# Optimization experiments

Hardware: AMD Instinct MI355X
Metric: run time of the kernel (lower is better)

## Reference

```python
import jax, jax.numpy as jnp
import numpy as np

N_POS, D_MODEL, D_SAE, TOP_K = 2, 1024, 32768, 32


def setup_inputs() -> dict:
    key = jax.random.key(0)
    k_x, k_we, k_wd = jax.random.split(key, 3)
    x = jax.random.normal(k_x, (4096, N_POS, D_MODEL), dtype=jnp.float32)
    W_enc = jax.random.normal(k_we, (N_POS, D_MODEL, D_SAE), dtype=jnp.float32) * (1.0 / D_MODEL ** 0.5)
    W_dec = jax.random.normal(k_wd, (D_SAE, N_POS, D_MODEL), dtype=jnp.float32) * (1.0 / D_SAE ** 0.5)
    b_enc = jnp.zeros((D_SAE,), dtype=jnp.float32)
    b_dec = jnp.zeros((N_POS, D_MODEL), dtype=jnp.float32)
    return {"x": x, "W_enc": W_enc, "W_dec": W_dec, "b_enc": b_enc, "b_dec": b_dec}


def reference(x, W_enc, W_dec, b_enc, b_dec):
    # Encode: per-position einsum then shared bias -> (batch, d_sae)
    pre_act = jnp.einsum('btd,tds->bs', x, W_enc) + b_enc
    top_vals, top_idx = jax.lax.top_k(pre_act, TOP_K)  # (b, k)
    batch = pre_act.shape[0]
    rows = jnp.arange(batch)[:, None]  # (b, 1) broadcast against (b, k)
    z = jnp.zeros_like(pre_act).at[rows, top_idx].set(jax.nn.relu(top_vals))
    # Decode: dense contraction over d_sae -> (batch, n_positions, d_model)
    x_hat = jnp.einsum('bs,std->btd', z, W_dec) + b_dec
    return x_hat
```

## Files before the change

kernel.cpp:

```cpp
#include <hip/hip_runtime.h>
#include <cstdint>
#include <cstddef>

typedef unsigned short u16;
typedef unsigned long long u64;
typedef __attribute__((ext_vector_type(8))) short short8;
typedef __attribute__((ext_vector_type(4))) float f32x4;

constexpr int K_DIM = 2048;
constexpr int S_DIM = 32768;
constexpr int TOPK  = 32;
constexpr int CAP   = 256;
#define EPS      0.06f
#define THR_EMIT 3.7f
#define HIST_LO  3.5f

__device__ __forceinline__ u16 f2bf(float f) {
    unsigned u = __float_as_uint(f);
    return (u16)((u + 0x7FFFu + ((u >> 16) & 1u)) >> 16);
}
__device__ __forceinline__ unsigned key_map(float f) {
    unsigned u = __float_as_uint(f);
    return (u & 0x80000000u) ? ~u : (u | 0x80000000u);
}
__device__ __forceinline__ float key_unmap(unsigned k) {
    unsigned u = (k & 0x80000000u) ? (k ^ 0x80000000u) : ~k;
    return __uint_as_float(u);
}

__global__ __launch_bounds__(256) void init_kernel(int* __restrict__ flag, int M)
{
    int i = blockIdx.x * 256 + threadIdx.x;
    if (i < M) flag[i] = 0;
}

__global__ __launch_bounds__(256) void conv_x_kernel(
    const float* __restrict__ x, u16* __restrict__ hi, int n4)
{
    int i = blockIdx.x * 256 + threadIdx.x;
    if (i >= n4) return;
    float4 v = ((const float4*)x)[i];
    ushort4 h;
    h.x = f2bf(v.x); h.y = f2bf(v.y); h.z = f2bf(v.z); h.w = f2bf(v.w);
    ((ushort4*)hi)[i] = h;
}

__global__ __launch_bounds__(256) void conv_wt_kernel(
    const float* __restrict__ W, float* __restrict__ WT, u16* __restrict__ Wh)
{
    __shared__ float tile[64][65];
    const int t  = threadIdx.x;
    const int s0 = blockIdx.x * 64;
    const int k0 = blockIdx.y * 64;
#pragma unroll
    for (int i = 0; i < 4; ++i) {
        int kl = (t >> 4) + i * 16;
        int sc = (t & 15) * 4;
        float4 v = *(const float4*)&W[(size_t)(k0 + kl) * S_DIM + s0 + sc];
        tile[kl][sc] = v.x; tile[kl][sc + 1] = v.y;
        tile[kl][sc + 2] = v.z; tile[kl][sc + 3] = v.w;
    }
    __syncthreads();
    const int klc = (t & 7) * 8;
#pragma unroll
    for (int i = 0; i < 2; ++i) {
        int sl = (t >> 3) + i * 32;
        float f[8];
        short8 h8;
#pragma unroll
        for (int j = 0; j < 8; ++j) {
            f[j] = tile[klc + j][sl];
            h8[j] = (short)f2bf(f[j]);
        }
        size_t o = (size_t)(s0 + sl) * K_DIM + k0 + klc;
        *(float4*)&WT[o]     = make_float4(f[0], f[1], f[2], f[3]);
        *(float4*)&WT[o + 4] = make_float4(f[4], f[5], f[6], f[7]);
        *(short8*)&Wh[o] = h8;
    }
}

__device__ __forceinline__ void gl16(const u16* g, u16* s) {
    __builtin_amdgcn_global_load_lds(
        (const __attribute__((address_space(1))) unsigned int*)g,
        (__attribute__((address_space(3))) unsigned int*)s,
        16, 0, 0);
}

#define LGKM0  do { asm volatile("s_waitcnt lgkmcnt(0)" ::: "memory"); \
                    __builtin_amdgcn_sched_barrier(0); } while (0)
#define VMW(n) asm volatile("s_waitcnt vmcnt(" #n ")" ::: "memory")
#define BAR    do { __builtin_amdgcn_s_barrier(); \
                    __builtin_amdgcn_sched_barrier(0); } while (0)

__global__ __launch_bounds__(512, 2) void gemm_mfma_kernel(
    const u16* __restrict__ A, const u16* __restrict__ B,
    const float* __restrict__ bias, float* __restrict__ C)
{
    __shared__ alignas(16) u16 sA[2][256 * 64];
    __shared__ alignas(16) u16 sB[2][256 * 64];

    const int t = threadIdx.x;
    const int lane = t & 63;
    const int w = t >> 6;
    const int wm = w >> 2, wn = w & 3;

    const int nwg = gridDim.x;
    const int q = nwg >> 3;
    const int bid = blockIdx.x;
    const int wg = (bid & 7) * q + (bid >> 3);
    const int bm = wg >> 7;
    const int bn = wg & 127;

    const u16* Ab = A + (size_t)bm * 256 * K_DIM;
    const u16* Bb = B + (size_t)bn * 256 * K_DIM;

    const int w2  = w * 2;
    const int lr3 = lane >> 3;
    const int csw = ((lane & 7) ^ lr3) * 8;

    const int rl = lane & 15, kq = lane >> 4;
    const int swz = rl & 7;
    const int ac0 = (kq ^ swz) * 8;
    const int ac1 = ((4 + kq) ^ swz) * 8;
    const int arow = (wm * 16 + rl) * 64;
    const int brow = (wn * 16 + rl) * 64;

    f32x4 acc[8][4];
#pragma unroll
    for (int m = 0; m < 8; ++m)
#pragma unroll
        for (int n = 0; n < 4; ++n) acc[m][n] = (f32x4){0.f, 0.f, 0.f, 0.f};

    auto stA = [&](int half, int j, int kt, int buf) {
        const u16* src = Ab + (size_t)(half * 128 + (w2 + j) * 8 + lr3) * K_DIM
                            + kt * 64 + csw;
        gl16(src, &sA[buf][half * 8192 + (w2 + j) * 512]);
    };
    auto stB = [&](int half, int j, int kt, int buf) {
        const u16* src = Bb + (size_t)(half * 128 + (w2 + j) * 8 + lr3) * K_DIM
                            + kt * 64 + csw;
        gl16(src, &sB[buf][half * 8192 + (w2 + j) * 512]);
    };

    stA(0, 0, 0, 0); stA(0, 1, 0, 0);
    stB(0, 0, 0, 0); stB(0, 1, 0, 0);
    stB(1, 0, 0, 0); stB(1, 1, 0, 0);
    stA(1, 0, 0, 0); stA(1, 1, 0, 0);
    VMW(4);
    BAR;

    short8 af[4][2], bf[4][2];

#pragma unroll 1
    for (int kt = 0; kt < 32; ++kt) {
        const int cur = kt & 1, nxt = cur ^ 1;
        const bool more = (kt < 31);

#pragma unroll
        for (int m = 0; m < 4; ++m) {
            af[m][0] = *(const short8*)&sA[cur][arow + m * 2048 + ac0];
            af[m][1] = *(const short8*)&sA[cur][arow + m * 2048 + ac1];
        }
#pragma unroll
        for (int n = 0; n < 2; ++n) {
            bf[n][0] = *(const short8*)&sB[cur][brow + n * 4096 + ac0];
            bf[n][1] = *(const short8*)&sB[cur][brow + n * 4096 + ac1];
        }
        if (more) { stA(0, 0, kt + 1, nxt); stA(0, 1, kt + 1, nxt); }
        __builtin_amdgcn_s_barrier();
        LGKM0;
        __builtin_amdgcn_s_setprio(1);
#pragma unroll
        for (int m = 0; m < 4; ++m)
#pragma unroll
            for (int n = 0; n < 2; ++n)
#pragma unroll
                for (int kk = 0; kk < 2; ++kk)
                    acc[m][n] = __builtin_amdgcn_mfma_f32_16x16x32_bf16(
                        af[m][kk], bf[n][kk], acc[m][n], 0, 0, 0);
        __builtin_amdgcn_s_setprio(0);
        if (more) VMW(4); else VMW(2);
        BAR;

#pragma unroll
        for (int n = 2; n < 4; ++n) {
            bf[n][0] = *(const short8*)&sB[cur][brow + n * 4096 + ac0];
            bf[n][1] = *(const short8*)&sB[cur][brow + n * 4096 + ac1];
        }
        if (more) { stB(0, 0, kt + 1, nxt); stB(0, 1, kt + 1, nxt); }
        __builtin_amdgcn_s_barrier();
        LGKM0;
        __builtin_amdgcn_s_setprio(1);
#pragma unroll
        for (int m = 0; m < 4; ++m)
#pragma unroll
            for (int n = 2; n < 4; ++n)
#pragma unroll
                for (int kk = 0; kk < 2; ++kk)
                    acc[m][n] = __builtin_amdgcn_mfma_f32_16x16x32_bf16(
                        af[m][kk], bf[n][kk], acc[m][n], 0, 0, 0);
        __builtin_amdgcn_s_setprio(0);
        if (more) VMW(4); else VMW(0);
        BAR;

#pragma unroll
        for (int m = 0; m < 4; ++m) {
            af[m][0] = *(const short8*)&sA[cur][arow + (m + 4) * 2048 + ac0];
            af[m][1] = *(const short8*)&sA[cur][arow + (m + 4) * 2048 + ac1];
        }
        if (more) { stB(1, 0, kt + 1, nxt); stB(1, 1, kt + 1, nxt); }
        __builtin_amdgcn_s_barrier();
        LGKM0;
        __builtin_amdgcn_s_setprio(1);
#pragma unroll
        for (int m = 0; m < 4; ++m)
#pragma unroll
            for (int n = 2; n < 4; ++n)
#pragma unroll
                for (int kk = 0; kk < 2; ++kk)
                    acc[m + 4][n] = __builtin_amdgcn_mfma_f32_16x16x32_bf16(
                        af[m][kk], bf[n][kk], acc[m + 4][n], 0, 0, 0);
        __builtin_amdgcn_s_setprio(0);
        BAR;

        if (more) { stA(1, 0, kt + 1, nxt); stA(1, 1, kt + 1, nxt); }
        __builtin_amdgcn_s_barrier();
        __builtin_amdgcn_s_setprio(1);
#pragma unroll
        for (int m = 0; m < 4; ++m)
#pragma unroll
            for (int n = 0; n < 2; ++n)
#pragma unroll
                for (int kk = 0; kk < 2; ++kk)
                    acc[m + 4][n] = __builtin_amdgcn_mfma_f32_16x16x32_bf16(
                        af[m][kk], bf[n][kk], acc[m + 4][n], 0, 0, 0);
        __builtin_amdgcn_s_setprio(0);
        if (more) VMW(4);
        BAR;
    }

    const int colB = bn * 256 + wn * 16 + rl;
    const size_t rowB = (size_t)bm * 256 + wm * 16 + kq * 4;
    float bv[4];
#pragma unroll
    for (int n = 0; n < 4; ++n) bv[n] = bias[colB + n * 64];
#pragma unroll
    for (int m = 0; m < 8; ++m)
#pragma unroll
        for (int n = 0; n < 4; ++n)
#pragma unroll
            for (int rr = 0; rr < 4; ++rr)
                C[(rowB + m * 32 + rr) * S_DIM + colB + n * 64] =
                    acc[m][n][rr] + bv[n];
}

__global__ __launch_bounds__(256) void screen_kernel(
    const float* __restrict__ pre, u64* __restrict__ emit,
    int* __restrict__ ccnt, float* __restrict__ thrv,
    int* __restrict__ flag, int row0)
{
    __shared__ unsigned hist[64];
    __shared__ int cnt;

    const int t = threadIdx.x;
    const int row = blockIdx.x;
    const int grow = row0 + row;
    const float* prow = pre + (size_t)row * S_DIM;

    if (t < 64) hist[t] = 0;
    if (t == 0) cnt = 0;
    __syncthreads();

    u64* erow = emit + (size_t)grow * CAP;
    for (int i = t * 4; i < S_DIM; i += 1024) {
        float4 v = *(const float4*)(prow + i);
        float vv[4] = {v.x, v.y, v.z, v.w};
#pragma unroll
        for (int j = 0; j < 4; ++j) {
            if (vv[j] >= HIST_LO) {
                int b = (int)((vv[j] - HIST_LO) * 25.0f);
                if (b > 63) b = 63;
                atomicAdd(&hist[b], 1u);
                if (vv[j] >= THR_EMIT) {
                    int p = atomicAdd(&cnt, 1);
                    if (p < CAP)
                        erow[p] = ((u64)key_map(vv[j]) << 32) | (unsigned)(i + j);
                }
            }
        }
    }
    __syncthreads();

    if (t == 0) {
        unsigned acc = 0;
        int b = -1;
        for (int j = 63; j >= 0; --j) {
            acc += hist[j];
            if (acc >= (unsigned)TOPK) { b = j; break; }
        }
        float thr = HIST_LO + 0.04f * b - 2.0f * EPS - 1e-4f;
        if (b < 0 || cnt > CAP || thr < THR_EMIT) {
            flag[grow] = 1;
            thr = THR_EMIT;
        }
        thrv[grow] = thr;
        ccnt[grow] = (cnt < CAP) ? cnt : CAP;
    }
}

__global__ __launch_bounds__(256) void rescore_kernel(
    const float* __restrict__ x, const float* __restrict__ WT,
    const float* __restrict__ benc, const u64* __restrict__ emit,
    const int* __restrict__ ccnt, const float* __restrict__ thrv,
    float* __restrict__ resc, int row0)
{
    const int row = row0 + blockIdx.x;
    const int t = threadIdx.x;
    const int w = t >> 6, l = t & 63;
    const int cnt = ccnt[row];
    const float thr = thrv[row];

    __shared__ float xs[K_DIM];
    const float* xr = x + (size_t)row * K_DIM;
    for (int i = t * 4; i < K_DIM; i += 1024)
        *(float4*)&xs[i] = *(const float4*)&xr[i];
    __syncthreads();

    for (int c = w; c < cnt; c += 4) {
        const u64 pk = emit[(size_t)row * CAP + c];
        const float approx = key_unmap((unsigned)(pk >> 32));
        if (approx < thr) {
            if (l == 0) resc[(size_t)row * CAP + c] = -3e38f;
            continue;
        }
        const int s = (int)(pk & 0xFFFFFFFFu);
        const float* wc = WT + (size_t)s * K_DIM;
        float acc = 0.f;
#pragma unroll
        for (int j = 0; j < 32; ++j)
            acc = fmaf(xs[l + 64 * j], wc[l + 64 * j], acc);
#pragma unroll
        for (int d = 1; d < 64; d <<= 1) acc += __shfl_xor(acc, d);
        if (l == 0) resc[(size_t)row * CAP + c] = acc + benc[s];
    }
}

__global__ __launch_bounds__(64) void select_kernel(
    const float* __restrict__ resc, const u64* __restrict__ emit,
    const int* __restrict__ ccnt, const float* __restrict__ thrv,
    float* __restrict__ tv, int* __restrict__ ti, int* __restrict__ flag,
    int row0)
{
    const int row = row0 + blockIdx.x;
    const int l = threadIdx.x;
    const int cnt = ccnt[row];

    float v[4] = {0.f, 0.f, 0.f, 0.f};
    int   s[4] = {-1, -1, -1, -1};
    u64   p[4] = {0, 0, 0, 0};
#pragma unroll
    for (int j = 0; j < 4; ++j) {
        int c = l + j * 64;
        if (c < cnt) {
            s[j] = (int)(emit[(size_t)row * CAP + c] & 0xFFFFFFFFu);
            v[j] = resc[(size_t)row * CAP + c];
            p[j] = ((u64)key_map(v[j]) << 32) | (unsigned)(~s[j]);
        }
    }

    float* tvr = tv + (size_t)row * TOPK;
    int*   tir = ti + (size_t)row * TOPK;
    float v32f = -3e38f;
#pragma unroll 1
    for (int r = 0; r < TOPK; ++r) {
        u64 m = p[0];
        if (p[1] > m) m = p[1];
        if (p[2] > m) m = p[2];
        if (p[3] > m) m = p[3];
#pragma unroll
        for (int d = 1; d < 64; d <<= 1) {
            u64 o = __shfl_xor(m, d);
            if (o > m) m = o;
        }
        if (r == TOPK - 1) v32f = key_unmap((unsigned)(m >> 32));
        if (p[0] == m)      { tvr[r] = v[0]; tir[r] = s[0] < 0 ? 0 : s[0]; p[0] = 0; }
        else if (p[1] == m) { tvr[r] = v[1]; tir[r] = s[1] < 0 ? 0 : s[1]; p[1] = 0; }
        else if (p[2] == m) { tvr[r] = v[2]; tir[r] = s[2] < 0 ? 0 : s[2]; p[2] = 0; }
        else if (p[3] == m) { tvr[r] = v[3]; tir[r] = s[3] < 0 ? 0 : s[3]; p[3] = 0; }
    }
    if (l == 0) {
        if (v32f < thrv[row] + EPS) flag[row] = 1;
    }
}

__global__ __launch_bounds__(256) void fb_screen_kernel(
    const float* __restrict__ pre, u64* __restrict__ emit,
    int* __restrict__ ccnt, const int* __restrict__ flag, int row0)
{
    const int grow = row0 + blockIdx.x;
    if (!flag[grow]) return;

    __shared__ unsigned hist[2048];
    __shared__ unsigned partial[256];
    __shared__ unsigned sh_tk;
    __shared__ int cnt;

    const int t = threadIdx.x;
    const float* prow = pre + (size_t)blockIdx.x * S_DIM;

    for (int i = t; i < 2048; i += 256) hist[i] = 0;
    if (t == 0) cnt = 0;
    __syncthreads();

    for (int i = t * 4; i < S_DIM; i += 1024) {
        float4 v = *(const float4*)(prow + i);
        unsigned k0 = key_map(v.x), k1 = key_map(v.y),
                 k2 = key_map(v.z), k3 = key_map(v.w);
        if (k0 >= 0xC0000000u) atomicAdd(&hist[(k0 >> 19) - 6144], 1u);
        if (k1 >= 0xC0000000u) atomicAdd(&hist[(k1 >> 19) - 6144], 1u);
        if (k2 >= 0xC0000000u) atomicAdd(&hist[(k2 >> 19) - 6144], 1u);
        if (k3 >= 0xC0000000u) atomicAdd(&hist[(k3 >> 19) - 6144], 1u);
    }
    __syncthreads();

    unsigned ps = 0;
#pragma unroll
    for (int j = 0; j < 8; ++j) ps += hist[t * 8 + j];
    partial[t] = ps;
    __syncthreads();

    if (t == 0) {
        unsigned acc = 0;
        int seg = -1;
        for (int s = 255; s >= 0; --s) {
            if (acc + partial[s] >= (unsigned)TOPK) { seg = s; break; }
            acc += partial[s];
        }
        int bucket = 6144;
        if (seg >= 0) {
            for (int b = seg * 8 + 7; b >= seg * 8; --b) {
                acc += hist[b];
                if (acc >= (unsigned)TOPK) { bucket = 6144 + b; break; }
            }
        }
        float lo = key_unmap(((unsigned)bucket) << 19) - 2.0f * EPS;
        sh_tk = key_map(lo);
    }
    __syncthreads();

    const unsigned TK = sh_tk;
    u64* erow = emit + (size_t)grow * CAP;
    for (int i = t * 4; i < S_DIM; i += 1024) {
        float4 v = *(const float4*)(prow + i);
        unsigned k[4] = {key_map(v.x), key_map(v.y), key_map(v.z), key_map(v.w)};
#pragma unroll
        for (int j = 0; j < 4; ++j)
            if (k[j] >= TK) {
                int p = atomicAdd(&cnt, 1);
                if (p < CAP) erow[p] = ((u64)k[j] << 32) | (unsigned)(i + j);
            }
    }
    __syncthreads();
    if (t == 0) ccnt[grow] = (cnt < CAP) ? cnt : CAP;
}

__global__ __launch_bounds__(256) void fb_rescore_kernel(
    const float* __restrict__ x, const float* __restrict__ WT,
    const float* __restrict__ benc, const u64* __restrict__ emit,
    const int* __restrict__ ccnt, float* __restrict__ resc,
    const int* __restrict__ flag, int row0)
{
    const int row = row0 + blockIdx.x;
    if (!flag[row]) return;
    const int t = threadIdx.x;
    const int w = t >> 6, l = t & 63;
    const int cnt = ccnt[row];

    __shared__ float xs[K_DIM];
    const float* xr = x + (size_t)row * K_DIM;
    for (int i = t * 4; i < K_DIM; i += 1024)
        *(float4*)&xs[i] = *(const float4*)&xr[i];
    __syncthreads();

    for (int c = w; c < cnt; c += 4) {
        const int s = (int)(emit[(size_t)row * CAP + c] & 0xFFFFFFFFu);
        const float* wc = WT + (size_t)s * K_DIM;
        float acc = 0.f;
#pragma unroll
        for (int j = 0; j < 32; ++j)
            acc = fmaf(xs[l + 64 * j], wc[l + 64 * j], acc);
#pragma unroll
        for (int d = 1; d < 64; d <<= 1) acc += __shfl_xor(acc, d);
        if (l == 0) resc[(size_t)row * CAP + c] = acc + benc[s];
    }
}

__global__ __launch_bounds__(64) void fb_select_kernel(
    const float* __restrict__ resc, const u64* __restrict__ emit,
    const int* __restrict__ ccnt, float* __restrict__ tv,
    int* __restrict__ ti, const int* __restrict__ flag, int row0)
{
    const int row = row0 + blockIdx.x;
    if (!flag[row]) return;
    const int l = threadIdx.x;
    const int cnt = ccnt[row];

    float v[4] = {0.f, 0.f, 0.f, 0.f};
    int   s[4] = {-1, -1, -1, -1};
    u64   p[4] = {0, 0, 0, 0};
#pragma unroll
    for (int j = 0; j < 4; ++j) {
        int c = l + j * 64;
        if (c < cnt) {
            s[j] = (int)(emit[(size_t)row * CAP + c] & 0xFFFFFFFFu);
            v[j] = resc[(size_t)row * CAP + c];
            p[j] = ((u64)key_map(v[j]) << 32) | (unsigned)(~s[j]);
        }
    }

    float* tvr = tv + (size_t)row * TOPK;
    int*   tir = ti + (size_t)row * TOPK;
#pragma unroll 1
    for (int r = 0; r < TOPK; ++r) {
        u64 m = p[0];
        if (p[1] > m) m = p[1];
        if (p[2] > m) m = p[2];
        if (p[3] > m) m = p[3];
#pragma unroll
        for (int d = 1; d < 64; d <<= 1) {
            u64 o = __shfl_xor(m, d);
            if (o > m) m = o;
        }
        if (p[0] == m)      { tvr[r] = v[0]; tir[r] = s[0] < 0 ? 0 : s[0]; p[0] = 0; }
        else if (p[1] == m) { tvr[r] = v[1]; tir[r] = s[1] < 0 ? 0 : s[1]; p[1] = 0; }
        else if (p[2] == m) { tvr[r] = v[2]; tir[r] = s[2] < 0 ? 0 : s[2]; p[2] = 0; }
        else if (p[3] == m) { tvr[r] = v[3]; tir[r] = s[3] < 0 ? 0 : s[3]; p[3] = 0; }
    }
}

__global__ __launch_bounds__(256) void decode_kernel(
    const float* __restrict__ tval, const int* __restrict__ tidx,
    const float* __restrict__ Wd, const float* __restrict__ bdec,
    float* __restrict__ out, int row0)
{
    const int row = row0 + blockIdx.x;
    const int t = threadIdx.x;
    __shared__ float sv[TOPK];
    __shared__ int   si[TOPK];
    if (t < TOPK) {
        sv[t] = fmaxf(tval[(size_t)row * TOPK + t], 0.f);
        si[t] = tidx[(size_t)row * TOPK + t];
    }
    __syncthreads();

    const int c0 = t * 4;
    float4 acc0 = *(const float4*)(bdec + c0);
    float4 acc1 = *(const float4*)(bdec + 1024 + c0);
#pragma unroll 4
    for (int i = 0; i < TOPK; ++i) {
        const float z = sv[i];
        if (z > 0.f) {
            const float* wr = Wd + (size_t)si[i] * K_DIM;
            float4 w0 = *(const float4*)(wr + c0);
            float4 w1 = *(const float4*)(wr + 1024 + c0);
            acc0.x = fmaf(z, w0.x, acc0.x); acc0.y = fmaf(z, w0.y, acc0.y);
            acc0.z = fmaf(z, w0.z, acc0.z); acc0.w = fmaf(z, w0.w, acc0.w);
            acc1.x = fmaf(z, w1.x, acc1.x); acc1.y = fmaf(z, w1.y, acc1.y);
            acc1.z = fmaf(z, w1.z, acc1.z); acc1.w = fmaf(z, w1.w, acc1.w);
        }
    }
    float* op = out + (size_t)row * K_DIM;
    *(float4*)(op + c0) = acc0;
    *(float4*)(op + 1024 + c0) = acc1;
}

extern "C" void kernel_launch(void* const* d_in, const int* in_sizes, int n_in,
                              void* d_out, int out_size, void* d_ws, size_t ws_size,
                              hipStream_t stream)
{
    const float* x     = (const float*)d_in[0];
    const float* W_enc = (const float*)d_in[1];
    const float* W_dec = (const float*)d_in[2];
    const float* b_enc = (const float*)d_in[3];
    const float* b_dec = (const float*)d_in[4];
    float* out = (float*)d_out;

    const int M = in_sizes[0] / K_DIM;

    char* wsb = (char*)d_ws;
    size_t o = 0;
    float*    tv   = (float*)(wsb + o);    o += (size_t)M * TOPK * 4;
    int*      ti   = (int*)(wsb + o);      o += (size_t)M * TOPK * 4;
    u64*      emit = (u64*)(wsb + o);      o += (size_t)M * CAP * 8;
    int*      ccnt = (int*)(wsb + o);      o += (size_t)M * 4;
    float*    thrv = (float*)(wsb + o);    o += (size_t)M * 4;
    int*      flag = (int*)(wsb + o);      o += (size_t)M * 4;
    float*    resc = (float*)(wsb + o);    o += (size_t)M * CAP * 4;
    u16*      Xh   = (u16*)(wsb + o);      o += (size_t)M * K_DIM * 2;
    u16*      Wh   = (u16*)(wsb + o);      o += (size_t)S_DIM * K_DIM * 2;
    float*    WT   = (float*)(wsb + o);    o += (size_t)S_DIM * K_DIM * 4;
    float*    pre  = (float*)(wsb + o);

    size_t cap = (ws_size > o) ? (ws_size - o) : 0;
    long cap_rows = (long)(cap / ((size_t)S_DIM * 4));
    int chunk = (int)((cap_rows / 256) * 256);
    if (chunk <= 0) chunk = 256;
    if (chunk > M) chunk = M;

    init_kernel<<<(M + 255) / 256, 256, 0, stream>>>(flag, M);
    const int n4 = M * K_DIM / 4;
    conv_x_kernel<<<(n4 + 255) / 256, 256, 0, stream>>>(x, Xh, n4);
    conv_wt_kernel<<<dim3(S_DIM / 64, K_DIM / 64), 256, 0, stream>>>(W_enc, WT, Wh);

    for (int r0 = 0; r0 < M; r0 += chunk) {
        const int rows = (M - r0 < chunk) ? (M - r0) : chunk;
        const int nbm = rows / 256;
        gemm_mfma_kernel<<<nbm * 128, 512, 0, stream>>>(
            Xh + (size_t)r0 * K_DIM, Wh, b_enc, pre);
        screen_kernel<<<rows, 256, 0, stream>>>(pre, emit, ccnt, thrv, flag, r0);
        rescore_kernel<<<rows, 256, 0, stream>>>(x, WT, b_enc, emit, ccnt, thrv, resc, r0);
        select_kernel<<<rows, 64, 0, stream>>>(resc, emit, ccnt, thrv, tv, ti, flag, r0);
        fb_screen_kernel<<<rows, 256, 0, stream>>>(pre, emit, ccnt, flag, r0);
        fb_rescore_kernel<<<rows, 256, 0, stream>>>(x, WT, b_enc, emit, ccnt, resc, flag, r0);
        fb_select_kernel<<<rows, 64, 0, stream>>>(resc, emit, ccnt, tv, ti, flag, r0);
        decode_kernel<<<rows, 256, 0, stream>>>(tv, ti, W_dec, b_dec, out, r0);
    }
}
```

Measured before the change: 1.295 ms.

## Deepen encoder GEMM prefetch to span tiles across LDS halves

Restructures the bf16 MFMA encoder GEMM main loop so that the global-to-LDS loads for a tile go out further ahead. Quarter-tiles of the next K-slab are written into the opposite or same buffer as soon as their previous contents are consumed. The prologue preloads tile 0 plus three quarters of tile 1, and the loop is unrolled by two so buffer indices are compile-time. This keeps more loads in flight (vmcnt 6 instead of 4) to hide global memory latency, at the cost of a trickier buffer-reuse ordering that must be correct under the barriers.

```diff
diff --git a/kernel.cpp b/kernel.cpp
--- a/kernel.cpp
+++ b/kernel.cpp
@@ -142,101 +142,107 @@
         gl16(src, &sB[buf][half * 8192 + (w2 + j) * 512]);
     };
 
+    stB(0, 0, 0, 0); stB(0, 1, 0, 0);
     stA(0, 0, 0, 0); stA(0, 1, 0, 0);
-    stB(0, 0, 0, 0); stB(0, 1, 0, 0);
     stB(1, 0, 0, 0); stB(1, 1, 0, 0);
     stA(1, 0, 0, 0); stA(1, 1, 0, 0);
-    VMW(4);
+    stB(0, 0, 1, 1); stB(0, 1, 1, 1);
+    stA(0, 0, 1, 1); stA(0, 1, 1, 1);
+    stB(1, 0, 1, 1); stB(1, 1, 1, 1);
+    VMW(6);
     BAR;
 
     short8 af[4][2], bf[4][2];
 
 #pragma unroll 1
-    for (int kt = 0; kt < 32; ++kt) {
-        const int cur = kt & 1, nxt = cur ^ 1;
-        const bool more = (kt < 31);
-
-#pragma unroll
-        for (int m = 0; m < 4; ++m) {
-            af[m][0] = *(const short8*)&sA[cur][arow + m * 2048 + ac0];
-            af[m][1] = *(const short8*)&sA[cur][arow + m * 2048 + ac1];
-        }
-#pragma unroll
-        for (int n = 0; n < 2; ++n) {
-            bf[n][0] = *(const short8*)&sB[cur][brow + n * 4096 + ac0];
-            bf[n][1] = *(const short8*)&sB[cur][brow + n * 4096 + ac1];
-        }
-        if (more) { stA(0, 0, kt + 1, nxt); stA(0, 1, kt + 1, nxt); }
-        __builtin_amdgcn_s_barrier();
-        LGKM0;
-        __builtin_amdgcn_s_setprio(1);
-#pragma unroll
-        for (int m = 0; m < 4; ++m)
-#pragma unroll
-            for (int n = 0; n < 2; ++n)
-#pragma unroll
-                for (int kk = 0; kk < 2; ++kk)
-                    acc[m][n] = __builtin_amdgcn_mfma_f32_16x16x32_bf16(
-                        af[m][kk], bf[n][kk], acc[m][n], 0, 0, 0);
-        __builtin_amdgcn_s_setprio(0);
-        if (more) VMW(4); else VMW(2);
-        BAR;
-
-#pragma unroll
-        for (int n = 2; n < 4; ++n) {
-            bf[n][0] = *(const short8*)&sB[cur][brow + n * 4096 + ac0];
-            bf[n][1] = *(const short8*)&sB[cur][brow + n * 4096 + ac1];
-        }
-        if (more) { stB(0, 0, kt + 1, nxt); stB(0, 1, kt + 1, nxt); }
-        __builtin_amdgcn_s_barrier();
-        LGKM0;
-        __builtin_amdgcn_s_setprio(1);
-#pragma unroll
-        for (int m = 0; m < 4; ++m)
-#pragma unroll
-            for (int n = 2; n < 4; ++n)
-#pragma unroll
-                for (int kk = 0; kk < 2; ++kk)
-                    acc[m][n] = __builtin_amdgcn_mfma_f32_16x16x32_bf16(
-                        af[m][kk], bf[n][kk], acc[m][n], 0, 0, 0);
-        __builtin_amdgcn_s_setprio(0);
-        if (more) VMW(4); else VMW(0);
-        BAR;
-
-#pragma unroll
-        for (int m = 0; m < 4; ++m) {
-            af[m][0] = *(const short8*)&sA[cur][arow + (m + 4) * 2048 + ac0];
-            af[m][1] = *(const short8*)&sA[cur][arow + (m + 4) * 2048 + ac1];
-        }
-        if (more) { stB(1, 0, kt + 1, nxt); stB(1, 1, kt + 1, nxt); }
-        __builtin_amdgcn_s_barrier();
-        LGKM0;
-        __builtin_amdgcn_s_setprio(1);
-#pragma unroll
-        for (int m = 0; m < 4; ++m)
-#pragma unroll
-            for (int n = 2; n < 4; ++n)
-#pragma unroll
-                for (int kk = 0; kk < 2; ++kk)
-                    acc[m + 4][n] = __builtin_amdgcn_mfma_f32_16x16x32_bf16(
-                        af[m][kk], bf[n][kk], acc[m + 4][n], 0, 0, 0);
-        __builtin_amdgcn_s_setprio(0);
-        BAR;
-
-        if (more) { stA(1, 0, kt + 1, nxt); stA(1, 1, kt + 1, nxt); }
-        __builtin_amdgcn_s_barrier();
-        __builtin_amdgcn_s_setprio(1);
-#pragma unroll
-        for (int m = 0; m < 4; ++m)
-#pragma unroll
-            for (int n = 0; n < 2; ++n)
-#pragma unroll
-                for (int kk = 0; kk < 2; ++kk)
-                    acc[m + 4][n] = __builtin_amdgcn_mfma_f32_16x16x32_bf16(
-                        af[m][kk], bf[n][kk], acc[m + 4][n], 0, 0, 0);
-        __builtin_amdgcn_s_setprio(0);
-        if (more) VMW(4);
-        BAR;
+    for (int it = 0; it < 16; ++it) {
+        const bool lastIt = (it == 15);
+#pragma unroll
+        for (int h = 0; h < 2; ++h) {
+            const int b  = h;
+            const int tA = 2 * it + 1 + h;
+            const int tB = 2 * it + 2 + h;
+
+#pragma unroll
+            for (int m = 0; m < 4; ++m) {
+                af[m][0] = *(const short8*)&sA[b][arow + m * 2048 + ac0];
+                af[m][1] = *(const short8*)&sA[b][arow + m * 2048 + ac1];
+            }
+#pragma unroll
+            for (int n = 0; n < 2; ++n) {
+                bf[n][0] = *(const short8*)&sB[b][brow + n * 4096 + ac0];
+                bf[n][1] = *(const short8*)&sB[b][brow + n * 4096 + ac1];
+            }
+            if (tA < 32) { stA(1, 0, tA, b ^ 1); stA(1, 1, tA, b ^ 1); }
+            __builtin_amdgcn_s_barrier();
+            LGKM0;
+            __builtin_amdgcn_s_setprio(1);
+#pragma unroll
+            for (int m = 0; m < 4; ++m)
+#pragma unroll
+                for (int n = 0; n < 2; ++n)
+#pragma unroll
+                    for (int kk = 0; kk < 2; ++kk)
+                        acc[m][n] = __builtin_amdgcn_mfma_f32_16x16x32_bf16(
+                            af[m][kk], bf[n][kk], acc[m][n], 0, 0, 0);
+            __builtin_amdgcn_s_setprio(0);
+            BAR;
+
+#pragma unroll
+            for (int n = 2; n < 4; ++n) {
+                bf[n][0] = *(const short8*)&sB[b][brow + n * 4096 + ac0];
+                bf[n][1] = *(const short8*)&sB[b][brow + n * 4096 + ac1];
+            }
+            if (tB < 32) { stB(0, 0, tB, b); stB(0, 1, tB, b); }
+            __builtin_amdgcn_s_barrier();
+            LGKM0;
+            __builtin_amdgcn_s_setprio(1);
+#pragma unroll
+            for (int m = 0; m < 4; ++m)
+#pragma unroll
+                for (int n = 2; n < 4; ++n)
+#pragma unroll
+                    for (int kk = 0; kk < 2; ++kk)
+                        acc[m][n] = __builtin_amdgcn_mfma_f32_16x16x32_bf16(
+                            af[m][kk], bf[n][kk], acc[m][n], 0, 0, 0);
+            __builtin_amdgcn_s_setprio(0);
+            BAR;
+
+#pragma unroll
+            for (int m = 0; m < 4; ++m) {
+                af[m][0] = *(const short8*)&sA[b][arow + (m + 4) * 2048 + ac0];
+                af[m][1] = *(const short8*)&sA[b][arow + (m + 4) * 2048 + ac1];
+            }
+            if (tB < 32) { stA(0, 0, tB, b); stA(0, 1, tB, b); }
+            __builtin_amdgcn_s_barrier();
+            LGKM0;
+            __builtin_amdgcn_s_setprio(1);
+#pragma unroll
+            for (int m = 0; m < 4; ++m)
+#pragma unroll
+                for (int n = 2; n < 4; ++n)
+#pragma unroll
+                    for (int kk = 0; kk < 2; ++kk)
+                        acc[m + 4][n] = __builtin_amdgcn_mfma_f32_16x16x32_bf16(
+                            af[m][kk], bf[n][kk], acc[m + 4][n], 0, 0, 0);
+            __builtin_amdgcn_s_setprio(0);
+            BAR;
+
+            if (tB < 32) { stB(1, 0, tB, b); stB(1, 1, tB, b); }
+            __builtin_amdgcn_s_barrier();
+            __builtin_amdgcn_s_setprio(1);
+#pragma unroll
+            for (int m = 0; m < 4; ++m)
+#pragma unroll
+                for (int n = 0; n < 2; ++n)
+#pragma unroll
+                    for (int kk = 0; kk < 2; ++kk)
+                        acc[m + 4][n] = __builtin_amdgcn_mfma_f32_16x16x32_bf16(
+                            af[m][kk], bf[n][kk], acc[m + 4][n], 0, 0, 0);
+            __builtin_amdgcn_s_setprio(0);
+            if (lastIt && h == 0) { VMW(0); } else { VMW(6); }
+            BAR;
+        }
     }
 
     const int colB = bn * 256 + wn * 16 + rl;
```

New measurement: 1.234 ms. -4.7%, faster.
